# Performance work log

Hardware: AMD Instinct MI355X
Metric: run time of the kernel (lower is better)

Reference implementation:

```python
import jax, jax.numpy as jnp
import numpy as np
from jax import lax

F_, W_, H_ = -0.01, -0.1, 1.0
K5 = np.array([[F_]*5, [F_, W_, W_, W_, F_], [F_, W_, H_, W_, F_], [F_, W_, W_, W_, F_], [F_]*5], dtype=np.float32)
K3 = np.array([[W_, W_, W_], [W_, H_, W_], [W_, W_, W_]], dtype=np.float32)


def depthwise_conv(x, k2d):
    # x: [B,C,H,W]; same small kernel applied independently to every channel
    C = x.shape[1]
    kh = k2d.shape[0]
    kernel = jnp.broadcast_to(jnp.asarray(k2d, x.dtype)[None, None], (C, 1, kh, kh))
    pad = kh // 2
    return lax.conv_general_dilated(
        x, kernel,
        window_strides=(1, 1),
        padding=[(pad, pad), (pad, pad)],
        dimension_numbers=("NCHW", "OIHW", "NCHW"),
        feature_group_count=C,
    )


def maxpool5(x):
    # kernel_size=5, stride=1, padding=2 (torch MaxPool2d pads with -inf)
    return lax.reduce_window(
        x, -jnp.inf, lax.max,
        window_dimensions=(1, 1, 5, 5),
        window_strides=(1, 1, 1, 1),
        padding=[(0, 0), (0, 0), (2, 2), (2, 2)],
    )


def setup_inputs() -> dict:
    key = jax.random.key(0)
    x = jax.random.normal(key, (8, 64, 256, 256), dtype=jnp.float32)
    return {"x": x}


def reference(x):
    edge = depthwise_conv(x, K5) + depthwise_conv(x, K3)
    return jnp.abs(maxpool5(edge))
```

## Files before the change

kernel.cpp:

```cpp
#include <hip/hip_runtime.h>
#include <math.h>


#define TY 8
#define STEPS (TY + 8)

typedef float vfloat4 __attribute__((ext_vector_type(4)));

__global__ __launch_bounds__(256, 4)
void edgepool_kernel(const float* __restrict__ xin, float* __restrict__ yout) {
    const int lane  = threadIdx.x & 63;
    const int wave  = threadIdx.x >> 6;
    const int blk   = blockIdx.x;
    const int plane = blk >> 3;
    const int strip = ((blk & 7) << 2) | wave;
    const int y0    = strip * TY;

    const float4* __restrict__ in4  = (const float4*)xin + (size_t)plane * 16384;
    vfloat4*      __restrict__ out4 = (vfloat4*)    yout + (size_t)plane * 16384;

    const float Wa = -0.01f, Wb = -0.19f, Wc = 2.2f;
    const float NINF = -INFINITY;

    float4 pf[STEPS];
#pragma unroll
    for (int t = 0; t < STEPS; ++t) {
        const int r  = y0 - 4 + t;
        const int rc = (r < 0) ? 0 : (r > 255 ? 255 : r);
        pf[t] = in4[rc * 64 + lane];
    }

    float E[5][4];
    float V[5][4];
#pragma unroll
    for (int k = 0; k < 5; ++k)
#pragma unroll
        for (int j = 0; j < 4; ++j) { E[k][j] = 0.f; V[k][j] = NINF; }

#pragma unroll
    for (int t = 0; t < STEPS; ++t) {
        const int  r   = y0 - 4 + t;
        const bool rin = (unsigned)r < 256u;
        const float v0 = rin ? pf[t].x : 0.f;
        const float v1 = rin ? pf[t].y : 0.f;
        const float v2 = rin ? pf[t].z : 0.f;
        const float v3 = rin ? pf[t].w : 0.f;

        float lm2 = __shfl(v2, lane - 1, 64);
        float lm1 = __shfl(v3, lane - 1, 64);
        float rp0 = __shfl(v0, lane + 1, 64);
        float rp1 = __shfl(v1, lane + 1, 64);
        lm2 = (lane == 0)  ? 0.f : lm2;
        lm1 = (lane == 0)  ? 0.f : lm1;
        rp0 = (lane == 63) ? 0.f : rp0;
        rp1 = (lane == 63) ? 0.f : rp1;

        const float s01 = v0 + v1, s23 = v2 + v3;
        const float h3[4] = { lm1 + s01, s01 + v2, v1 + s23, s23 + rp0 };
        const float h5[4] = { lm2 + lm1 + s01 + v2, lm1 + s01 + s23,
                              s01 + s23 + rp0,      v1 + s23 + rp0 + rp1 };
        const float vv[4] = { v0, v1, v2, v3 };

        const int e2 = (t + 2) % 5, e1 = (t + 1) % 5, e0 = t % 5,
                  em1 = (t + 4) % 5, em2 = (t + 3) % 5;

#pragma unroll
        for (int j = 0; j < 4; ++j) {
            E[e2][j]  = Wa * h5[j];
            E[e1][j]  = fmaf(Wb, h3[j], fmaf(Wa, h5[j], E[e1][j]));
            E[e0][j]  = fmaf(Wc, vv[j], fmaf(Wb, h3[j], fmaf(Wa, h5[j], E[e0][j])));
            E[em1][j] = fmaf(Wb, h3[j], fmaf(Wa, h5[j], E[em1][j]));
            E[em2][j] = fmaf(Wa, h5[j], E[em2][j]);
        }

        const int  er  = r - 2;
        const bool ein = (unsigned)er < 256u;
        float e[4];
#pragma unroll
        for (int j = 0; j < 4; ++j) e[j] = ein ? E[em2][j] : NINF;

#pragma unroll
        for (int j = 0; j < 4; ++j) {
            V[e2][j]  = e[j];
            V[e1][j]  = fmaxf(V[e1][j], e[j]);
            V[e0][j]  = fmaxf(V[e0][j], e[j]);
            V[em1][j] = fmaxf(V[em1][j], e[j]);
            V[em2][j] = fmaxf(V[em2][j], e[j]);
        }

        if (t >= 8) {
            const float m0 = V[em2][0], m1 = V[em2][1], m2 = V[em2][2], m3 = V[em2][3];
            float ml2 = __shfl(m2, lane - 1, 64);
            float ml1 = __shfl(m3, lane - 1, 64);
            float mr0 = __shfl(m0, lane + 1, 64);
            float mr1 = __shfl(m1, lane + 1, 64);
            ml2 = (lane == 0)  ? NINF : ml2;
            ml1 = (lane == 0)  ? NINF : ml1;
            mr0 = (lane == 63) ? NINF : mr0;
            mr1 = (lane == 63) ? NINF : mr1;
            vfloat4 ov;
            ov.x = fabsf(fmaxf(fmaxf(ml2, ml1), fmaxf(fmaxf(m0, m1), m2)));
            ov.y = fabsf(fmaxf(fmaxf(ml1, m0), fmaxf(fmaxf(m1, m2), m3)));
            ov.z = fabsf(fmaxf(fmaxf(m0, m1), fmaxf(fmaxf(m2, m3), mr0)));
            ov.w = fabsf(fmaxf(fmaxf(m1, m2), fmaxf(fmaxf(m3, mr0), mr1)));
            __builtin_nontemporal_store(ov, &out4[(r - 4) * 64 + lane]);
        }
    }
}

extern "C" void kernel_launch(void* const* d_in, const int* in_sizes, int n_in,
                              void* d_out, int out_size, void* d_ws, size_t ws_size,
                              hipStream_t stream) {
    const float* x   = (const float*)d_in[0];
    float*       out = (float*)d_out;
    hipLaunchKernelGGL(edgepool_kernel, dim3(4096), dim3(256), 0, stream, x, out);
}
```

Before: 231.4 us.

## Stage input strip in LDS shared across waves instead of per-wave register prefetch

Each block now loads a 40-row halo strip (32 output rows plus 4-row halos) into shared memory once, with zero padding for the horizontal borders. Each wave then reads its 16 rows from LDS, taking the left and right neighbours directly instead of using cross-lane shuffles. This lowers redundant global halo reads (previously each wave loaded 16 rows for 8 outputs) and removes the input shuffles. In exchange it adds a __syncthreads and about 42KB of LDS per block, and the launch bound drops to 3 blocks per SM.

```diff
diff --git a/kernel.cpp b/kernel.cpp
--- a/kernel.cpp
+++ b/kernel.cpp
@@ -2,33 +2,41 @@
 #include <math.h>
 
 
-#define TY 8
-#define STEPS (TY + 8)
+#define STRIP   32
+#define HALO    4
+#define SROWS   (STRIP + 2*HALO)
+#define RSTRIDE 264
 
 typedef float vfloat4 __attribute__((ext_vector_type(4)));
 
-__global__ __launch_bounds__(256, 4)
+__global__ __launch_bounds__(256, 3)
 void edgepool_kernel(const float* __restrict__ xin, float* __restrict__ yout) {
     const int lane  = threadIdx.x & 63;
     const int wave  = threadIdx.x >> 6;
     const int blk   = blockIdx.x;
     const int plane = blk >> 3;
-    const int strip = ((blk & 7) << 2) | wave;
-    const int y0    = strip * TY;
+    const int strip = blk & 7;
+    const int y0    = strip * STRIP;
 
     const float4* __restrict__ in4  = (const float4*)xin + (size_t)plane * 16384;
     vfloat4*      __restrict__ out4 = (vfloat4*)    yout + (size_t)plane * 16384;
 
+    __shared__ float tile[SROWS * RSTRIDE];
+
+#pragma unroll
+    for (int k = 0; k < 10; ++k) {
+        const int lr = wave + 4 * k;
+        const int r  = y0 - HALO + lr;
+        float4 v = make_float4(0.f, 0.f, 0.f, 0.f);
+        if ((unsigned)r < 256u) v = in4[r * 64 + lane];
+        *(float4*)&tile[lr * RSTRIDE + 4 + 4 * lane] = v;
+        if (lane < 4)
+            tile[lr * RSTRIDE + ((lane < 2) ? 2 + lane : 258 + lane)] = 0.f;
+    }
+    __syncthreads();
+
     const float Wa = -0.01f, Wb = -0.19f, Wc = 2.2f;
     const float NINF = -INFINITY;
-
-    float4 pf[STEPS];
-#pragma unroll
-    for (int t = 0; t < STEPS; ++t) {
-        const int r  = y0 - 4 + t;
-        const int rc = (r < 0) ? 0 : (r > 255 ? 255 : r);
-        pf[t] = in4[rc * 64 + lane];
-    }
 
     float E[5][4];
     float V[5][4];
@@ -38,22 +46,15 @@
         for (int j = 0; j < 4; ++j) { E[k][j] = 0.f; V[k][j] = NINF; }
 
 #pragma unroll
-    for (int t = 0; t < STEPS; ++t) {
-        const int  r   = y0 - 4 + t;
-        const bool rin = (unsigned)r < 256u;
-        const float v0 = rin ? pf[t].x : 0.f;
-        const float v1 = rin ? pf[t].y : 0.f;
-        const float v2 = rin ? pf[t].z : 0.f;
-        const float v3 = rin ? pf[t].w : 0.f;
+    for (int t = 0; t < 16; ++t) {
+        const int lr = 8 * wave + t;
+        const int r  = y0 - HALO + lr;
 
-        float lm2 = __shfl(v2, lane - 1, 64);
-        float lm1 = __shfl(v3, lane - 1, 64);
-        float rp0 = __shfl(v0, lane + 1, 64);
-        float rp1 = __shfl(v1, lane + 1, 64);
-        lm2 = (lane == 0)  ? 0.f : lm2;
-        lm1 = (lane == 0)  ? 0.f : lm1;
-        rp0 = (lane == 63) ? 0.f : rp0;
-        rp1 = (lane == 63) ? 0.f : rp1;
+        const float2* p = (const float2*)&tile[lr * RSTRIDE + 2 + 4 * lane];
+        const float2 A = p[0], B = p[1], C = p[2], D = p[3];
+        const float lm2 = A.x, lm1 = A.y;
+        const float v0 = B.x, v1 = B.y, v2 = C.x, v3 = C.y;
+        const float rp0 = D.x, rp1 = D.y;
 
         const float s01 = v0 + v1, s23 = v2 + v3;
         const float h3[4] = { lm1 + s01, s01 + v2, v1 + s23, s23 + rp0 };
```

Measured after the change: 238.2 us. 2.9% more time.
